# Kernel optimization log

Hardware: AMD Instinct MI355X
Metric: run time of the kernel (lower is better)

Reference implementation:

```python
import jax, jax.numpy as jnp
import numpy as np

B, L, D = 2, 8192, 768
F = 768          # features
ORDER = 2
MAX_LEN = 8192
POS_DIM = 8
INNER = F * (ORDER + 1)  # 2304


def sine_pos_embedding(seq_len, dim=POS_DIM, max_seq_len=MAX_LEN):
    # sine_lin: linearly spaced periods, wrap to negative offsets, include linear coord
    offset = jnp.arange(seq_len)
    offset = jnp.concatenate([offset, offset - seq_len])          # [2L]
    periods = jnp.linspace(4.0, float(max_seq_len), dim // 2)
    freqs = 2.0 * jnp.pi / periods
    phases = jnp.outer(offset, freqs)                              # [2L, dim/2]
    pos_emb = jnp.concatenate((jnp.cos(phases), jnp.sin(phases)), axis=-1)
    pos_emb = jnp.concatenate((offset[:, None] / max_seq_len, pos_emb), axis=-1)
    return pos_emb  # [2L, dim+1]


def fftconv(v, h, bias):
    # v: [B, L, F], h: [1, 2L, F], bias: [1, 1, F]
    seqlen = v.shape[-2]
    n = 2 * seqlen
    h_f = jnp.fft.rfft(h, n=n, axis=-2)
    v_f = jnp.fft.rfft(v, n=n, axis=-2)
    y_f = v_f * h_f / n
    y = jnp.fft.irfft(y_f, axis=-2, n=n, norm='forward')[:, :seqlen, :]
    return y + v * bias


def setup_inputs() -> dict:
    key = jax.random.key(0)
    ks = jax.random.split(key, 13)
    inp = {
        'u': jax.random.normal(ks[0], (B, L, D), jnp.float32),
        'filter_w1': jax.random.normal(ks[1], (POS_DIM + 1, 64), jnp.float32) * (1.0 / np.sqrt(POS_DIM + 1)),
        'filter_b1': jnp.zeros((64,), jnp.float32),
        'filter_w2': jax.random.normal(ks[2], (64, ORDER * F), jnp.float32) * (1.0 / np.sqrt(64)),
        'filter_b2': jnp.zeros((ORDER * F,), jnp.float32),
        'decay': jax.random.uniform(ks[3], (ORDER, F), jnp.float32, 0.5, 4.0),
        'bias': jax.random.normal(ks[4], (ORDER, 1, 1, F), jnp.float32),  # bias_init=1
        'in_proj_w': jax.random.normal(ks[5], (D, INNER), jnp.float32) * 0.02,
        'in_proj_b': jnp.zeros((INNER,), jnp.float32),
        'short_w': jax.random.normal(ks[6], (3, 1, INNER), jnp.float32) * 0.02,  # grouped conv, groups=INNER
        'short_b': jnp.zeros((INNER,), jnp.float32),
        'out_w': jax.random.normal(ks[7], (F, D), jnp.float32) * (1.0 / np.sqrt(F)),
        'out_b': jnp.zeros((D,), jnp.float32),
    }
    return inp


def reference(u, filter_w1, filter_b1, filter_w2, filter_b2, decay, bias,
              in_proj_w, in_proj_b, short_w, short_b, out_w, out_b):
    seq_len = u.shape[-2]
    # --- implicit filter generation from positional embedding ---
    t = sine_pos_embedding(seq_len)[None, :, :]                    # [1, 2L, 9]
    h = jnp.sin(t @ filter_w1 + filter_b1) @ filter_w2 + filter_b2 # [1, 2L, ORDER*F]
    h = h.reshape(1, 2 * seq_len, ORDER, F)
    # --- modulation: exponential decay over normalized position ---
    mod_t = jnp.linspace(0.0, 1.0, MAX_LEN)[:seq_len]
    mod_t = jnp.concatenate([mod_t, jnp.flip(mod_t)])[None, :, None, None]  # [1, 2L, 1, 1]
    h = h * jnp.exp(-mod_t * jnp.abs(decay)[None, None, :, :])
    h = jnp.transpose(h, (2, 0, 1, 3))                             # [ORDER, 1, 2L, F]
    # --- input projection ---
    u = u @ in_proj_w + in_proj_b                                  # [B, L, INNER]
    # --- grouped short conv (depthwise, k=3, SAME) ---
    u = jax.lax.conv_general_dilated(
        u, short_w, window_strides=(1,), padding='SAME',
        dimension_numbers=('NWC', 'WIO', 'NWC'),
        feature_group_count=INNER) + short_b
    # --- hyena recurrence: v <- gate(fftconv(v)) ---
    splits = jnp.split(u, ORDER + 1, axis=-1)
    v, x = splits[0], splits[1:]
    for o in range(ORDER):
        v = fftconv(v, h[o], bias[o])
        v = v * x[o]
    # --- output projection ---
    y = v @ out_w + out_b
    return y
```

## Files before the change

### kernel.cpp

```cpp
#include <hip/hip_runtime.h>
#include <hip/hip_bf16.h>
#include <math.h>

#define L_SEQ 8192
#define NFFT  16384
#define NPAD  16896
#define F_DIM 768
#define D_DIM 768
#define C_IN  2304
#define NORD  2
#define NT    512
#define TWO_PI 6.2831853071795864769f

typedef unsigned short u16;
typedef __attribute__((ext_vector_type(8))) short bf16x8;
typedef __attribute__((ext_vector_type(4))) float f32x4;
struct __align__(8) U16x4 { u16 x, y, z, w; };

__device__ __forceinline__ float bf2f(u16 v) {
  unsigned u = ((unsigned)v) << 16; float f; __builtin_memcpy(&f, &u, 4); return f;
}
__device__ __forceinline__ u16 f2bf(float f) {
  __hip_bfloat16 h = __float2bfloat16(f); u16 r; __builtin_memcpy(&r, &h, 2); return r;
}

__device__ __forceinline__ int PAD(int i) { return i + (i >> 5); }

__device__ __forceinline__ int rev4_14(int p) {
  return ((p & 0x0003) << 12) | ((p & 0x000C) << 8) | ((p & 0x0030) << 4)
       | ( p & 0x00C0       ) | ((p & 0x0300) >> 4) | ((p & 0x0C00) >> 8)
       | ((p & 0x3000) >> 12);
}

__device__ __forceinline__ void rot3(float ang, float& c1, float& s1,
                                     float& c2, float& s2, float& c3, float& s3)
{
  __sincosf(ang, &s1, &c1);
  c2 = c1 * c1 - s1 * s1; s2 = 2.0f * c1 * s1;
  c3 = c1 * c2 - s1 * s2; s3 = c1 * s2 + s1 * c2;
}

__device__ __forceinline__ float conv3b(const u16* __restrict__ row, int t,
                                        float w0, float w1, float w2, float sb)
{
  float l = (t > 0)         ? bf2f(row[t - 1]) : 0.0f;
  float c = bf2f(row[t]);
  float r = (t < L_SEQ - 1) ? bf2f(row[t + 1]) : 0.0f;
  return w0 * l + w1 * c + w2 * r + sb;
}


__device__ __forceinline__ void s1_l2_store(float* zr, float* zi, int g,
    const float yr[4][4], const float yi4[4][4])
{
  const float stw2 = -TWO_PI / 4096.0f;
  float c1, s1, c2, s2, c3, s3;
  rot3(stw2 * (float)g, c1, s1, c2, s2, c3, s3);
  #pragma unroll
  for (int k = 0; k < 4; ++k) {
    float t0r = yr[k][0] + yr[k][2], t0i = yi4[k][0] + yi4[k][2];
    float t1r = yr[k][0] - yr[k][2], t1i = yi4[k][0] - yi4[k][2];
    float t2r = yr[k][1] + yr[k][3], t2i = yi4[k][1] + yi4[k][3];
    float t3r = yr[k][1] - yr[k][3], t3i = yi4[k][1] - yi4[k][3];
    float o0r = t0r + t2r, o0i = t0i + t2i;
    float o1r = t1r + t3i, o1i = t1i - t3r;
    float o2r = t0r - t2r, o2i = t0i - t2i;
    float o3r = t1r - t3i, o3i = t1i + t3r;
    const int i0 = g + (k << 12);
    zr[PAD(i0       )] = o0r;               zi[PAD(i0       )] = o0i;
    zr[PAD(i0 + 1024)] = o1r*c1 - o1i*s1;   zi[PAD(i0 + 1024)] = o1r*s1 + o1i*c1;
    zr[PAD(i0 + 2048)] = o2r*c2 - o2i*s2;   zi[PAD(i0 + 2048)] = o2r*s2 + o2i*c2;
    zr[PAD(i0 + 3072)] = o3r*c3 - o3i*s3;   zi[PAD(i0 + 3072)] = o3r*s3 + o3i*c3;
  }
}

__device__ __forceinline__ void s1_zero_hi(float* zr, float* zi, int g,
    const float xr[2][4], const float xi[2][4])
{
  const float stw1 = -TWO_PI / 16384.0f;
  float yr[4][4], yi4[4][4];
  #pragma unroll
  for (int m = 0; m < 4; ++m) {
    const float x0r = xr[0][m], x0i = xi[0][m];
    const float x1r = xr[1][m], x1i = xi[1][m];
    const float y0r = x0r + x1r, y0i = x0i + x1i;
    const float y1r = x0r + x1i, y1i = x0i - x1r;
    const float y2r = x0r - x1r, y2i = x0i - x1i;
    const float y3r = x0r - x1i, y3i = x0i + x1r;
    float c1, s1, c2, s2, c3, s3;
    rot3(stw1 * (float)(g + (m << 10)), c1, s1, c2, s2, c3, s3);
    yr[0][m] = y0r;               yi4[0][m] = y0i;
    yr[1][m] = y1r*c1 - y1i*s1;   yi4[1][m] = y1r*s1 + y1i*c1;
    yr[2][m] = y2r*c2 - y2i*s2;   yi4[2][m] = y2r*s2 + y2i*c2;
    yr[3][m] = y3r*c3 - y3i*s3;   yi4[3][m] = y3r*s3 + y3i*c3;
  }
  s1_l2_store(zr, zi, g, yr, yi4);
}

template<int LQ0>
__device__ __forceinline__ void fwd_pairs(float* zr, float* zi, int tid)
{
  #pragma unroll
  for (int lq = LQ0; lq >= 4; lq -= 4) {
    const int q  = 1 << lq;
    const int q4 = q >> 2;
    const float stw1 = -TWO_PI / (float)(q << 2);
    const float stw2 = -TWO_PI / (float)q;
    for (int g = tid; g < NFFT / 16; g += NT) {
      const int j    = g & (q4 - 1);
      const int base = ((g >> (lq - 2)) << (lq + 2)) + j;
      float xr[4][4], xi4[4][4];
      #pragma unroll
      for (int k = 0; k < 4; ++k)
        #pragma unroll
        for (int m = 0; m < 4; ++m) {
          const int idx = PAD(base + m * q4 + k * q);
          xr[k][m] = zr[idx]; xi4[k][m] = zi[idx];
        }
      #pragma unroll
      for (int m = 0; m < 4; ++m) {
        float t0r = xr[0][m] + xr[2][m], t0i = xi4[0][m] + xi4[2][m];
        float t1r = xr[0][m] - xr[2][m], t1i = xi4[0][m] - xi4[2][m];
        float t2r = xr[1][m] + xr[3][m], t2i = xi4[1][m] + xi4[3][m];
        float t3r = xr[1][m] - xr[3][m], t3i = xi4[1][m] - xi4[3][m];
        float y0r = t0r + t2r, y0i = t0i + t2i;
        float y1r = t1r + t3i, y1i = t1i - t3r;
        float y2r = t0r - t2r, y2i = t0i - t2i;
        float y3r = t1r - t3i, y3i = t1i + t3r;
        float c1, s1, c2, s2, c3, s3;
        rot3(stw1 * (float)(j + m * q4), c1, s1, c2, s2, c3, s3);
        xr[0][m] = y0r;                xi4[0][m] = y0i;
        xr[1][m] = y1r * c1 - y1i * s1; xi4[1][m] = y1r * s1 + y1i * c1;
        xr[2][m] = y2r * c2 - y2i * s2; xi4[2][m] = y2r * s2 + y2i * c2;
        xr[3][m] = y3r * c3 - y3i * s3; xi4[3][m] = y3r * s3 + y3i * c3;
      }
      float c1, s1, c2, s2, c3, s3;
      rot3(stw2 * (float)j, c1, s1, c2, s2, c3, s3);
      #pragma unroll
      for (int k = 0; k < 4; ++k) {
        float t0r = xr[k][0] + xr[k][2], t0i = xi4[k][0] + xi4[k][2];
        float t1r = xr[k][0] - xr[k][2], t1i = xi4[k][0] - xi4[k][2];
        float t2r = xr[k][1] + xr[k][3], t2i = xi4[k][1] + xi4[k][3];
        float t3r = xr[k][1] - xr[k][3], t3i = xi4[k][1] - xi4[k][3];
        float y0r = t0r + t2r, y0i = t0i + t2i;
        float y1r = t1r + t3i, y1i = t1i - t3r;
        float y2r = t0r - t2r, y2i = t0i - t2i;
        float y3r = t1r - t3i, y3i = t1i + t3r;
        const int i0 = base + k * q;
        zr[PAD(i0         )] = y0r;            zi[PAD(i0         )] = y0i;
        zr[PAD(i0 +     q4)] = y1r*c1 - y1i*s1; zi[PAD(i0 +     q4)] = y1r*s1 + y1i*c1;
        zr[PAD(i0 + 2 * q4)] = y2r*c2 - y2i*s2; zi[PAD(i0 + 2 * q4)] = y2r*s2 + y2i*c2;
        zr[PAD(i0 + 3 * q4)] = y3r*c3 - y3i*s3; zi[PAD(i0 + 3 * q4)] = y3r*s3 + y3i*c3;
      }
    }
    __syncthreads();
  }
}

__device__ __forceinline__ void fused_final_spec_head(float* zr, float* zi,
    const __hip_bfloat162* __restrict__ H, int tid)
{
  for (int b = tid; b < NFFT / 4; b += NT) {
    const int i0 = b << 2;
    const int p  = PAD(i0);
    const float a0r = zr[p],     a0i = zi[p];
    const float a1r = zr[p + 1], a1i = zi[p + 1];
    const float a2r = zr[p + 2], a2i = zi[p + 2];
    const float a3r = zr[p + 3], a3i = zi[p + 3];
    float t0r = a0r + a2r, t0i = a0i + a2i;
    float t1r = a0r - a2r, t1i = a0i - a2i;
    float t2r = a1r + a3r, t2i = a1i + a3i;
    float t3r = a1r - a3r, t3i = a1i - a3i;
    float y0r = t0r + t2r, y0i = t0i + t2i;
    float y1r = t1r + t3i, y1i = t1i - t3r;
    float y2r = t0r - t2r, y2i = t0i - t2i;
    float y3r = t1r - t3i, y3i = t1i + t3r;
    const float4 hq = *(const float4*)&H[i0];
    __hip_bfloat162 h0, h1, h2, h3;
    __builtin_memcpy(&h0, &hq.x, 4); __builtin_memcpy(&h1, &hq.y, 4);
    __builtin_memcpy(&h2, &hq.z, 4); __builtin_memcpy(&h3, &hq.w, 4);
    float hr, hi;
    hr = __bfloat162float(h0.x); hi = __bfloat162float(h0.y);
    const float u0r = y0r*hr - y0i*hi, u0i = y0r*hi + y0i*hr;
    hr = __bfloat162float(h1.x); hi = __bfloat162float(h1.y);
    const float u1r = y1r*hr - y1i*hi, u1i = y1r*hi + y1i*hr;
    hr = __bfloat162float(h2.x); hi = __bfloat162float(h2.y);
    const float u2r = y2r*hr - y2i*hi, u2i = y2r*hi + y2i*hr;
    hr = __bfloat162float(h3.x); hi = __bfloat162float(h3.y);
    const float u3r = y3r*hr - y3i*hi, u3i = y3r*hi + y3i*hr;
    const float e0r = u0r + u2r, e0i = u0i + u2i;
    const float e1r = u0r - u2r, e1i = u0i - u2i;
    const float f0r = u1r + u3r, f0i = u1i + u3i;
    const float f1r = u1r - u3r, f1i = u1i - u3i;
    zr[p]     = e0r + f0r; zi[p]     = e0i + f0i;
    zr[p + 1] = e1r - f1i; zi[p + 1] = e1i + f1r;
    zr[p + 2] = e0r - f0r; zi[p + 2] = e0i - f0i;
    zr[p + 3] = e1r + f1i; zi[p + 3] = e1i - f1r;
  }
  __syncthreads();
}

__device__ __forceinline__ void inv_mid_pairs(float* zr, float* zi, int tid)
{
  #pragma unroll
  for (int lq = 2; lq <= 6; lq += 4) {
    const int q = 1 << lq;
    const int Q = q << 2;
    const float stw1 = TWO_PI / (float)(q << 2);
    const float stw2 = TWO_PI / (float)(Q << 2);
    for (int g = tid; g < NFFT / 16; g += NT) {
      const int j    = g & (q - 1);
      const int base = ((g >> lq) << (lq + 4)) + j;
      float xr[4][4], xi4[4][4];
      #pragma unroll
      for (int k = 0; k < 4; ++k)
        #pragma unroll
        for (int m = 0; m < 4; ++m) {
          const int idx = PAD(base + m * q + k * Q);
          xr[k][m] = zr[idx]; xi4[k][m] = zi[idx];
        }
      {
        float c1, s1, c2, s2, c3, s3;
        rot3(stw1 * (float)j, c1, s1, c2, s2, c3, s3);
        #pragma unroll
        for (int k = 0; k < 4; ++k) {
          float u0r = xr[k][0], u0i = xi4[k][0];
          float u1r = xr[k][1]*c1 - xi4[k][1]*s1, u1i = xr[k][1]*s1 + xi4[k][1]*c1;
          float u2r = xr[k][2]*c2 - xi4[k][2]*s2, u2i = xr[k][2]*s2 + xi4[k][2]*c2;
          float u3r = xr[k][3]*c3 - xi4[k][3]*s3, u3i = xr[k][3]*s3 + xi4[k][3]*c3;
          float e0r = u0r + u2r, e0i = u0i + u2i;
          float e1r = u0r - u2r, e1i = u0i - u2i;
          float f0r = u1r + u3r, f0i = u1i + u3i;
          float f1r = u1r - u3r, f1i = u1i - u3i;
          xr[k][0] = e0r + f0r; xi4[k][0] = e0i + f0i;
          xr[k][1] = e1r - f1i; xi4[k][1] = e1i + f1r;
          xr[k][2] = e0r - f0r; xi4[k][2] = e0i - f0i;
          xr[k][3] = e1r + f1i; xi4[k][3] = e1i - f1r;
        }
      }
      #pragma unroll
      for (int m = 0; m < 4; ++m) {
        float c1, s1, c2, s2, c3, s3;
        rot3(stw2 * (float)(j + m * q), c1, s1, c2, s2, c3, s3);
        float u0r = xr[0][m], u0i = xi4[0][m];
        float u1r = xr[1][m]*c1 - xi4[1][m]*s1, u1i = xr[1][m]*s1 + xi4[1][m]*c1;
        float u2r = xr[2][m]*c2 - xi4[2][m]*s2, u2i = xr[2][m]*s2 + xi4[2][m]*c2;
        float u3r = xr[3][m]*c3 - xi4[3][m]*s3, u3i = xr[3][m]*s3 + xi4[3][m]*c3;
        float e0r = u0r + u2r, e0i = u0i + u2i;
        float e1r = u0r - u2r, e1i = u0i - u2i;
        float f0r = u1r + u3r, f0i = u1i + u3i;
        float f1r = u1r - u3r, f1i = u1i - u3i;
        const int i0 = base + m * q;
        zr[PAD(i0        )] = e0r + f0r; zi[PAD(i0        )] = e0i + f0i;
        zr[PAD(i0 +     Q)] = e1r - f1i; zi[PAD(i0 +     Q)] = e1i + f1r;
        zr[PAD(i0 + 2 * Q)] = e0r - f0r; zi[PAD(i0 + 2 * Q)] = e0i - f0i;
        zr[PAD(i0 + 3 * Q)] = e1r + f1i; zi[PAD(i0 + 3 * Q)] = e1i - f1r;
      }
    }
    __syncthreads();
  }
}

template<bool TO_GLOBAL>
__device__ __forceinline__ void inv_last_gate(float* zr, float* zi,
    const u16* __restrict__ gr0, const u16* __restrict__ gr1,
    float w0, float w1, float w2, float wb, u16* __restrict__ outv, int tid)
{
  const float stw1 = TWO_PI / 4096.0f;
  const float stw2 = TWO_PI / 16384.0f;
  for (int g = tid; g < 1024; g += NT) {
    float xr[4][4], xi4[4][4];
    #pragma unroll
    for (int k = 0; k < 4; ++k)
      #pragma unroll
      for (int m = 0; m < 4; ++m) {
        const int idx = PAD(g + (m << 10) + (k << 12));
        xr[k][m] = zr[idx]; xi4[k][m] = zi[idx];
      }
    {
      float c1, s1, c2, s2, c3, s3;
      rot3(stw1 * (float)g, c1, s1, c2, s2, c3, s3);
      #pragma unroll
      for (int k = 0; k < 4; ++k) {
        float u0r = xr[k][0], u0i = xi4[k][0];
        float u1r = xr[k][1]*c1 - xi4[k][1]*s1, u1i = xr[k][1]*s1 + xi4[k][1]*c1;
        float u2r = xr[k][2]*c2 - xi4[k][2]*s2, u2i = xr[k][2]*s2 + xi4[k][2]*c2;
        float u3r = xr[k][3]*c3 - xi4[k][3]*s3, u3i = xr[k][3]*s3 + xi4[k][3]*c3;
        float e0r = u0r + u2r, e0i = u0i + u2i;
        float e1r = u0r - u2r, e1i = u0i - u2i;
        float f0r = u1r + u3r, f0i = u1i + u3i;
        float f1r = u1r - u3r, f1i = u1i - u3i;
        xr[k][0] = e0r + f0r; xi4[k][0] = e0i + f0i;
        xr[k][1] = e1r - f1i; xi4[k][1] = e1i + f1r;
        xr[k][2] = e0r - f0r; xi4[k][2] = e0i - f0i;
        xr[k][3] = e1r + f1i; xi4[k][3] = e1i - f1r;
      }
    }
    #pragma unroll
    for (int m = 0; m < 4; ++m) {
      float c1, s1, c2, s2, c3, s3;
      rot3(stw2 * (float)(g + (m << 10)), c1, s1, c2, s2, c3, s3);
      float u0r = xr[0][m], u0i = xi4[0][m];
      float u1r = xr[1][m]*c1 - xi4[1][m]*s1, u1i = xr[1][m]*s1 + xi4[1][m]*c1;
      float u2r = xr[2][m]*c2 - xi4[2][m]*s2, u2i = xr[2][m]*s2 + xi4[2][m]*c2;
      float u3r = xr[3][m]*c3 - xi4[3][m]*s3, u3i = xr[3][m]*s3 + xi4[3][m]*c3;
      float e0r = u0r + u2r, e0i = u0i + u2i;
      float e1r = u0r - u2r, e1i = u0i - u2i;
      float f0r = u1r + u3r, f0i = u1i + u3i;
      float f1r = u1r - u3r, f1i = u1i - u3i;
      const int t0 = g + (m << 10);
      const int t1 = t0 + 4096;
      const float o0r = e0r + f0r, o0i = e0i + f0i;
      const float o1r = e1r - f1i, o1i = e1i + f1r;
      const float a0 = conv3b(gr0, t0, w0, w1, w2, wb);
      const float b0 = conv3b(gr1, t0, w0, w1, w2, wb);
      const float a1 = conv3b(gr0, t1, w0, w1, w2, wb);
      const float b1 = conv3b(gr1, t1, w0, w1, w2, wb);
      if (TO_GLOBAL) {
        outv[t0]         = f2bf(o0r * a0);
        outv[L_SEQ + t0] = f2bf(o0i * b0);
        outv[t1]         = f2bf(o1r * a1);
        outv[L_SEQ + t1] = f2bf(o1i * b1);
      } else {
        zr[PAD(t0)] = o0r * a0;  zi[PAD(t0)] = o0i * b0;
        zr[PAD(t1)] = o1r * a1;  zi[PAD(t1)] = o1i * b1;
      }
    }
  }
  if (!TO_GLOBAL) __syncthreads();
}

__global__ __launch_bounds__(256)
void cast_bf16_kernel(const float* __restrict__ in, u16* __restrict__ out, int n4)
{
  int i = blockIdx.x * 256 + threadIdx.x;
  if (i < n4) {
    float4 v = ((const float4*)in)[i];
    U16x4 w; w.x = f2bf(v.x); w.y = f2bf(v.y); w.z = f2bf(v.z); w.w = f2bf(v.w);
    ((U16x4*)out)[i] = w;
  }
}

__global__ __launch_bounds__(256)
void transpose_cast_kernel(const float* __restrict__ in, u16* __restrict__ out,
                           int K, int N)
{
  __shared__ u16 tile[32][33];
  const int n0 = blockIdx.x * 32, k0 = blockIdx.y * 32;
  const int tx = threadIdx.x & 31, ty = threadIdx.x >> 5;
  #pragma unroll
  for (int i = 0; i < 32; i += 8)
    tile[ty + i][tx] = f2bf(in[(size_t)(k0 + ty + i) * N + n0 + tx]);
  __syncthreads();
  #pragma unroll
  for (int i = 0; i < 32; i += 8)
    out[(size_t)(n0 + ty + i) * K + k0 + tx] = tile[tx][ty + i];
}

__global__ __launch_bounds__(256)
void hid_gen_kernel(const float* __restrict__ w1, const float* __restrict__ b1,
                    u16* __restrict__ hidb)
{
  const int tid = threadIdx.x;
  const int r  = tid & 63;
  const int tb = tid >> 6;
  const float w1v0 = w1[r];
  const float b1v  = b1[r];
  float w1c[4], w1s[4];
  #pragma unroll
  for (int p = 0; p < 4; ++p) { w1c[p] = w1[(1 + p) * 64 + r]; w1s[p] = w1[(5 + p) * 64 + r]; }
  const int tau0 = blockIdx.x * 16;
  #pragma unroll
  for (int i = 0; i < 4; ++i) {
    const int tau = tau0 + tb + i * 4;
    const float off = (tau < L_SEQ) ? (float)tau : (float)(tau - NFFT);
    float acc = b1v + off * (1.0f / 8192.0f) * w1v0;
    #pragma unroll
    for (int p = 0; p < 4; ++p) {
      const double period = 4.0 + (8188.0 * p) / 3.0;
      const float freq = (float)(6.283185307179586476925287 / period);
      float sp, cp;
      sincosf(off * freq, &sp, &cp);
      acc += cp * w1c[p] + sp * w1s[p];
    }
    hidb[(size_t)tau * 64 + r] = f2bf(sinf(acc));
  }
}

template<int N_DIM, int K_DIM, int WMODE, int ATRANS = 0, int ASTR = 0>
__global__ __launch_bounds__(256)
void mfma_gemm_kernel(const u16* __restrict__ A, const u16* __restrict__ B,
                      const float* __restrict__ bias, void* __restrict__ Cv,
                      const float* __restrict__ dk)
{
  constexpr int BK = 64;
  __shared__ u16 As[128 * BK];
  __shared__ u16 Bs[128 * BK];
  const int tid  = threadIdx.x;
  const int lane = tid & 63;
  const int wid  = tid >> 6;
  const int m0 = blockIdx.x * 128;
  const int n0 = blockIdx.y * 128;

  const u16* aPtr[4]; const u16* bPtr[4];
  #pragma unroll
  for (int i = 0; i < 4; ++i) {
    const int g = tid + (i << 8);
    if (ATRANS == 0)
      aPtr[i] = A + (size_t)(m0 + (g >> 3)) * K_DIM + ((g & 7) << 3);
    bPtr[i] = B + (size_t)(n0 + (g >> 3)) * K_DIM + ((g & 7) << 3);
  }

  const int wm = (wid & 1) << 6;
  const int wn = (wid >> 1) << 6;
  int aoff[4], boff[4];
  #pragma unroll
  for (int f = 0; f < 4; ++f) {
    aoff[f] = (wm + f * 16 + (lane & 15)) * BK + ((lane >> 4) << 3);
    boff[f] = (wn + f * 16 + (lane & 15)) * BK + ((lane >> 4) << 3);
  }

  f32x4 acc[4][4];
  #pragma unroll
  for (int i = 0; i < 4; ++i)
    #pragma unroll
    for (int j = 0; j < 4; ++j)
      acc[i][j] = (f32x4){0.f, 0.f, 0.f, 0.f};

  for (int k0 = 0; k0 < K_DIM; k0 += BK) {
    if (ATRANS) {
      #pragma unroll
      for (int i = 0; i < 4; ++i) {
        const int g    = tid + (i << 8);
        const int krow = g & 63;
        const int mc   = g >> 6;
        const uint4 v = *(const uint4*)&A[(size_t)(k0 + krow) * ASTR + m0 + mc * 8];
        u16 e[8]; __builtin_memcpy(e, &v, 16);
        #pragma unroll
        for (int q = 0; q < 8; ++q)
          As[(mc * 8 + q) * BK + krow] = e[q];
      }
    } else {
      #pragma unroll
      for (int i = 0; i < 4; ++i) {
        __builtin_amdgcn_global_load_lds(
            (const __attribute__((address_space(1))) void*)aPtr[i],
            (__attribute__((address_space(3))) void*)&As[(((wid << 6) + (i << 8)) << 3)],
            16, 0, 0);
        aPtr[i] += BK;
      }
    }
    #pragma unroll
    for (int i = 0; i < 4; ++i) {
      __builtin_amdgcn_global_load_lds(
          (const __attribute__((address_space(1))) void*)bPtr[i],
          (__attribute__((address_space(3))) void*)&Bs[(((wid << 6) + (i << 8)) << 3)],
          16, 0, 0);
      bPtr[i] += BK;
    }
    __syncthreads();
    #pragma unroll
    for (int kk = 0; kk < 2; ++kk) {
      bf16x8 af[4], bg[4];
      #pragma unroll
      for (int f = 0; f < 4; ++f) af[f] = *(const bf16x8*)&As[aoff[f] + kk * 32];
      #pragma unroll
      for (int f = 0; f < 4; ++f) bg[f] = *(const bf16x8*)&Bs[boff[f] + kk * 32];
      #pragma unroll
      for (int fm = 0; fm < 4; ++fm)
        #pragma unroll
        for (int fn = 0; fn < 4; ++fn)
          acc[fm][fn] = __builtin_amdgcn_mfma_f32_16x16x32_bf16(
              af[fm], bg[fn], acc[fm][fn], 0, 0, 0);
    }
    __syncthreads();
  }

  if (WMODE == 0) {
    u16* C = (u16*)Cv;
    const int b = m0 >> 13;
    const int tbase = (m0 & (L_SEQ - 1)) + wm + ((lane >> 4) << 2);
    #pragma unroll
    for (int fn = 0; fn < 4; ++fn) {
      const int n = n0 + wn + fn * 16 + (lane & 15);
      const float bv = bias[n];
      u16* row = C + ((size_t)b * N_DIM + n) * L_SEQ;
      #pragma unroll
      for (int fm = 0; fm < 4; ++fm) {
        f32x4 v = acc[fm][fn];
        U16x4 w;
        w.x = f2bf(v[0] + bv); w.y = f2bf(v[1] + bv);
        w.z = f2bf(v[2] + bv); w.w = f2bf(v[3] + bv);
        *(U16x4*)&row[tbase + fm * 16] = w;
      }
    }
  } else if (WMODE == 1) {
    float* C = (float*)Cv;
    #pragma unroll
    for (int fn = 0; fn < 4; ++fn) {
      const int n = n0 + wn + fn * 16 + (lane & 15);
      const float bv = bias[n];
      #pragma unroll
      for (int fm = 0; fm < 4; ++fm) {
        const int mb = m0 + wm + fm * 16 + ((lane >> 4) << 2);
        f32x4 v = acc[fm][fn];
        #pragma unroll
        for (int r = 0; r < 4; ++r)
          C[(size_t)(mb + r) * N_DIM + n] = v[r] + bv;
      }
    }
  } else {
    u16* C = (u16*)Cv;
    #pragma unroll
    for (int fn = 0; fn < 4; ++fn) {
      const int n = n0 + wn + fn * 16 + (lane & 15);
      const float bv = bias[n];
      const float ad = fabsf(dk[n]);
      u16* row = C + (size_t)n * (2 * NFFT);
      #pragma unroll
      for (int fm = 0; fm < 4; ++fm) {
        const int mq = m0 + wm + fm * 16 + ((lane >> 4) << 2);
        f32x4 v = acc[fm][fn];
        U16x4 w;
        #pragma unroll
        for (int r = 0; r < 4; ++r) {
          const int t = mq + r;
          const float mt = (t < L_SEQ) ? (float)t * (1.0f / 8191.0f)
                                       : (float)(NFFT - 1 - t) * (1.0f / 8191.0f);
          const float dec = __expf(-mt * ad);
          ((u16*)&w)[r] = f2bf((v[r] + bv) * dec);
        }
        *(U16x4*)&row[mq] = w;
      }
    }
  }
}

__global__ __launch_bounds__(NT)
void filter_fft_kernel(float* __restrict__ hH, const float* __restrict__ bias)
{
  __shared__ float zr[NPAD];
  __shared__ float zi[NPAD];
  const int f = blockIdx.x;
  const int tid = threadIdx.x;
  float* row0 = hH + (size_t)f * NFFT;
  float* row1 = hH + (size_t)(F_DIM + f) * NFFT;
  const u16* h0 = (const u16*)row0;
  const u16* h1 = (const u16*)row1;

  for (int t = tid; t < NFFT; t += NT) {
    zr[PAD(t)] = bf2f(h0[t]);
    zi[PAD(t)] = bf2f(h1[t]);
  }
  __syncthreads();
  fwd_pairs<12>(zr, zi, tid);
  for (int b = tid; b < NFFT / 4; b += NT) {
    const int p = PAD(b << 2);
    const float a0r = zr[p],     a0i = zi[p];
    const float a1r = zr[p + 1], a1i = zi[p + 1];
    const float a2r = zr[p + 2], a2i = zi[p + 2];
    const float a3r = zr[p + 3], a3i = zi[p + 3];
    const float t0r = a0r + a2r, t0i = a0i + a2i;
    const float t1r = a0r - a2r, t1i = a0i - a2i;
    const float t2r = a1r + a3r, t2i = a1i + a3i;
    const float t3r = a1r - a3r, t3i = a1i - a3i;
    zr[p]     = t0r + t2r; zi[p]     = t0i + t2i;
    zr[p + 1] = t1r + t3i; zi[p + 1] = t1i - t3r;
    zr[p + 2] = t0r - t2r; zi[p + 2] = t0i - t2i;
    zr[p + 3] = t1r - t3i; zi[p + 3] = t1i + t3r;
  }
  __syncthreads();
  const float bo0 = bias[f];
  const float bo1 = bias[F_DIM + f];
  const float s = 1.0f / (float)NFFT;
  __hip_bfloat162* o0 = (__hip_bfloat162*)row0;
  __hip_bfloat162* o1 = (__hip_bfloat162*)row1;
  for (int p = tid; p < NFFT; p += NT) {
    const int k  = rev4_14(p);
    const int pb = rev4_14((NFFT - k) & (NFFT - 1));
    const float ar = zr[PAD(p)],  ai = zi[PAD(p)];
    const float br = zr[PAD(pb)], bi = zi[PAD(pb)];
    const float h0r = 0.5f * (ar + br), h0i = 0.5f * (ai - bi);
    const float h1r = 0.5f * (ai + bi), h1i = 0.5f * (br - ar);
    __hip_bfloat162 w0, w1;
    w0.x = __float2bfloat16((h0r + bo0) * s); w0.y = __float2bfloat16(h0i * s);
    w1.x = __float2bfloat16((h1r + bo1) * s); w1.y = __float2bfloat16(h1i * s);
    o0[p] = w0; o1[p] = w1;
  }
}

__global__ __launch_bounds__(NT)
void fftconv_kernel(const u16* __restrict__ up, float* __restrict__ hH,
                    const float* __restrict__ sw, const float* __restrict__ sb)
{
  __shared__ float zr[NPAD];
  __shared__ float zi[NPAD];
  const int f = blockIdx.x;
  const int tid = threadIdx.x;
  float* rowf = hH + (size_t)f * NFFT;
  float* row1 = hH + (size_t)(F_DIM + f) * NFFT;

  const u16* u0 = up + (size_t)(0 * C_IN + f) * L_SEQ;
  const u16* u1 = up + (size_t)(1 * C_IN + f) * L_SEQ;
  const float vw0 = sw[f], vw1 = sw[C_IN + f], vw2 = sw[2 * C_IN + f];
  const float vb = sb[f];

  for (int g = tid; g < 1024; g += NT) {
    float xr[2][4], xi[2][4];
    #pragma unroll
    for (int k = 0; k < 2; ++k)
      #pragma unroll
      for (int m = 0; m < 4; ++m) {
        const int t = g + (m << 10) + (k << 12);
        xr[k][m] = conv3b(u0, t, vw0, vw1, vw2, vb);
        xi[k][m] = conv3b(u1, t, vw0, vw1, vw2, vb);
      }
    s1_zero_hi(zr, zi, g, xr, xi);
  }
  __syncthreads();
  fwd_pairs<8>(zr, zi, tid);
  fused_final_spec_head(zr, zi, (const __hip_bfloat162*)rowf, tid);
  inv_mid_pairs(zr, zi, tid);

  const int c0g = F_DIM + f;
  inv_last_gate<false>(zr, zi,
      up + (size_t)(0 * C_IN + c0g) * L_SEQ,
      up + (size_t)(1 * C_IN + c0g) * L_SEQ,
      sw[c0g], sw[C_IN + c0g], sw[2 * C_IN + c0g], sb[c0g], nullptr, tid);

  for (int g = tid; g < 1024; g += NT) {
    float xr[2][4], xi[2][4];
    #pragma unroll
    for (int k = 0; k < 2; ++k)
      #pragma unroll
      for (int m = 0; m < 4; ++m) {
        const int idx = PAD(g + (m << 10) + (k << 12));
        xr[k][m] = zr[idx]; xi[k][m] = zi[idx];
      }
    s1_zero_hi(zr, zi, g, xr, xi);
  }
  __syncthreads();
  fwd_pairs<8>(zr, zi, tid);
  fused_final_spec_head(zr, zi, (const __hip_bfloat162*)row1, tid);
  inv_mid_pairs(zr, zi, tid);

  const int c1g = 2 * F_DIM + f;
  inv_last_gate<true>(zr, zi,
      up + (size_t)(0 * C_IN + c1g) * L_SEQ,
      up + (size_t)(1 * C_IN + c1g) * L_SEQ,
      sw[c1g], sw[C_IN + c1g], sw[2 * C_IN + c1g], sb[c1g], (u16*)rowf, tid);
}

extern "C" void kernel_launch(void* const* d_in, const int* in_sizes, int n_in,
                              void* d_out, int out_size, void* d_ws, size_t ws_size,
                              hipStream_t stream)
{
  (void)in_sizes; (void)n_in; (void)out_size; (void)ws_size;
  const float* u     = (const float*)d_in[0];
  const float* fw1   = (const float*)d_in[1];
  const float* fb1   = (const float*)d_in[2];
  const float* fw2   = (const float*)d_in[3];
  const float* fb2   = (const float*)d_in[4];
  const float* decay = (const float*)d_in[5];
  const float* bias  = (const float*)d_in[6];
  const float* ipw   = (const float*)d_in[7];
  const float* ipb   = (const float*)d_in[8];
  const float* sw    = (const float*)d_in[9];
  const float* sb    = (const float*)d_in[10];
  const float* ow    = (const float*)d_in[11];
  const float* ob    = (const float*)d_in[12];
  float* out = (float*)d_out;

  char* ws = (char*)d_ws;
  u16*   up_t  = (u16*)(ws);
  float* hH    = (float*)(ws + 75497472);
  u16*   u_bf  = (u16*)(ws + 176160768);
  u16*   ipw_t = (u16*)(ws + 201326592);
  u16*   ow_t  = (u16*)(ws + 204865536);
  u16*   hidb  = (u16*)(ws);
  u16*   w2t   = (u16*)(ws + 2097152);

  cast_bf16_kernel<<<dim3(12288), 256, 0, stream>>>(u, u_bf, (2 * L_SEQ * D_DIM) / 4);
  transpose_cast_kernel<<<dim3(C_IN / 32, D_DIM / 32), 256, 0, stream>>>(ipw, ipw_t, D_DIM, C_IN);
  transpose_cast_kernel<<<dim3(D_DIM / 32, F_DIM / 32), 256, 0, stream>>>(ow, ow_t, F_DIM, D_DIM);

  hid_gen_kernel<<<dim3(NFFT / 16), 256, 0, stream>>>(fw1, fb1, hidb);
  transpose_cast_kernel<<<dim3(1536 / 32, 64 / 32), 256, 0, stream>>>(fw2, w2t, 64, 1536);
  mfma_gemm_kernel<1536, 64, 2><<<dim3(NFFT / 128, 1536 / 128), 256, 0, stream>>>(
      hidb, w2t, fb2, hH, decay);
  filter_fft_kernel<<<dim3(F_DIM), NT, 0, stream>>>(hH, bias);

  mfma_gemm_kernel<C_IN, D_DIM, 0><<<dim3(128, C_IN / 128), 256, 0, stream>>>(u_bf, ipw_t, ipb, up_t, nullptr);
  fftconv_kernel<<<dim3(F_DIM), NT, 0, stream>>>(up_t, hH, sw, sb);
  mfma_gemm_kernel<D_DIM, F_DIM, 1, 1, 2 * NFFT><<<dim3(128, D_DIM / 128), 256, 0, stream>>>(
      (const u16*)hH, ow_t, ob, out, nullptr);
}
```

Baseline: 511.5 us.

## Use twiddle recurrence in FFT, swap GEMM grid order, pack transposed A stores

Several FFT radix stages now call __sincosf once per group and advance the twiddle for later sub-butterflies with a fixed 1/16-turn rotation, replacing three extra sincos calls. The GEMM kernel gains a GSWAP option that swaps the roles of blockIdx.x and blockIdx.y, so consecutive blocks walk the N tiles for the same M rows, aiming for better L2 reuse of A. The transposed-A load path now reads two K rows at once and writes packed 32-bit pairs to LDS, halving the number of LDS store instructions. The twiddle recurrence adds a small rounding drift across the four steps.

Measured after the change: 504.4 us. Within noise of the previous version (-1.4%).

```diff
diff --git a/kernel.cpp b/kernel.cpp
--- a/kernel.cpp
+++ b/kernel.cpp
@@ -11,6 +11,8 @@
 #define NORD  2
 #define NT    512
 #define TWO_PI 6.2831853071795864769f
+#define C16 0.92387953251128675613f
+#define S16 0.38268343236508977172f
 
 typedef unsigned short u16;
 typedef __attribute__((ext_vector_type(8))) short bf16x8;
@@ -38,6 +40,15 @@
   __sincosf(ang, &s1, &c1);
   c2 = c1 * c1 - s1 * s1; s2 = 2.0f * c1 * s1;
   c3 = c1 * c2 - s1 * s2; s3 = c1 * s2 + s1 * c2;
+}
+
+__device__ __forceinline__ void adv_fwd(float& c, float& s) {
+  const float cn = c * C16 + s * S16;
+  s = s * C16 - c * S16; c = cn;
+}
+__device__ __forceinline__ void adv_inv(float& c, float& s) {
+  const float cn = c * C16 - s * S16;
+  s = s * C16 + c * S16; c = cn;
 }
 
 __device__ __forceinline__ float conv3b(const u16* __restrict__ row, int t,
@@ -79,6 +90,8 @@
 {
   const float stw1 = -TWO_PI / 16384.0f;
   float yr[4][4], yi4[4][4];
+  float c1, s1;
+  __sincosf(stw1 * (float)g, &s1, &c1);
   #pragma unroll
   for (int m = 0; m < 4; ++m) {
     const float x0r = xr[0][m], x0i = xi[0][m];
@@ -87,12 +100,13 @@
     const float y1r = x0r + x1i, y1i = x0i - x1r;
     const float y2r = x0r - x1r, y2i = x0i - x1i;
     const float y3r = x0r - x1i, y3i = x0i + x1r;
-    float c1, s1, c2, s2, c3, s3;
-    rot3(stw1 * (float)(g + (m << 10)), c1, s1, c2, s2, c3, s3);
+    const float c2 = c1*c1 - s1*s1, s2 = 2.0f*c1*s1;
+    const float c3 = c1*c2 - s1*s2, s3 = c1*s2 + s1*c2;
     yr[0][m] = y0r;               yi4[0][m] = y0i;
     yr[1][m] = y1r*c1 - y1i*s1;   yi4[1][m] = y1r*s1 + y1i*c1;
     yr[2][m] = y2r*c2 - y2i*s2;   yi4[2][m] = y2r*s2 + y2i*c2;
     yr[3][m] = y3r*c3 - y3i*s3;   yi4[3][m] = y3r*s3 + y3i*c3;
+    adv_fwd(c1, s1);
   }
   s1_l2_store(zr, zi, g, yr, yi4);
 }
@@ -117,6 +131,8 @@
           const int idx = PAD(base + m * q4 + k * q);
           xr[k][m] = zr[idx]; xi4[k][m] = zi[idx];
         }
+      float c1a, s1a;
+      __sincosf(stw1 * (float)j, &s1a, &c1a);
       #pragma unroll
       for (int m = 0; m < 4; ++m) {
         float t0r = xr[0][m] + xr[2][m], t0i = xi4[0][m] + xi4[2][m];
@@ -127,12 +143,13 @@
         float y1r = t1r + t3i, y1i = t1i - t3r;
         float y2r = t0r - t2r, y2i = t0i - t2i;
         float y3r = t1r - t3i, y3i = t1i + t3r;
-        float c1, s1, c2, s2, c3, s3;
-        rot3(stw1 * (float)(j + m * q4), c1, s1, c2, s2, c3, s3);
-        xr[0][m] = y0r;                xi4[0][m] = y0i;
-        xr[1][m] = y1r * c1 - y1i * s1; xi4[1][m] = y1r * s1 + y1i * c1;
-        xr[2][m] = y2r * c2 - y2i * s2; xi4[2][m] = y2r * s2 + y2i * c2;
-        xr[3][m] = y3r * c3 - y3i * s3; xi4[3][m] = y3r * s3 + y3i * c3;
+        const float c2 = c1a*c1a - s1a*s1a, s2 = 2.0f*c1a*s1a;
+        const float c3 = c1a*c2 - s1a*s2, s3 = c1a*s2 + s1a*c2;
+        xr[0][m] = y0r;                  xi4[0][m] = y0i;
+        xr[1][m] = y1r * c1a - y1i * s1a; xi4[1][m] = y1r * s1a + y1i * c1a;
+        xr[2][m] = y2r * c2 - y2i * s2;   xi4[2][m] = y2r * s2 + y2i * c2;
+        xr[3][m] = y3r * c3 - y3i * s3;   xi4[3][m] = y3r * s3 + y3i * c3;
+        adv_fwd(c1a, s1a);
       }
       float c1, s1, c2, s2, c3, s3;
       rot3(stw2 * (float)j, c1, s1, c2, s2, c3, s3);
@@ -238,12 +255,14 @@
           xr[k][3] = e1r + f1i; xi4[k][3] = e1i - f1r;
         }
       }
+      float c1b, s1b;
+      __sincosf(stw2 * (float)j, &s1b, &c1b);
       #pragma unroll
       for (int m = 0; m < 4; ++m) {
-        float c1, s1, c2, s2, c3, s3;
-        rot3(stw2 * (float)(j + m * q), c1, s1, c2, s2, c3, s3);
+        const float c2 = c1b*c1b - s1b*s1b, s2 = 2.0f*c1b*s1b;
+        const float c3 = c1b*c2 - s1b*s2, s3 = c1b*s2 + s1b*c2;
         float u0r = xr[0][m], u0i = xi4[0][m];
-        float u1r = xr[1][m]*c1 - xi4[1][m]*s1, u1i = xr[1][m]*s1 + xi4[1][m]*c1;
+        float u1r = xr[1][m]*c1b - xi4[1][m]*s1b, u1i = xr[1][m]*s1b + xi4[1][m]*c1b;
         float u2r = xr[2][m]*c2 - xi4[2][m]*s2, u2i = xr[2][m]*s2 + xi4[2][m]*c2;
         float u3r = xr[3][m]*c3 - xi4[3][m]*s3, u3i = xr[3][m]*s3 + xi4[3][m]*c3;
         float e0r = u0r + u2r, e0i = u0i + u2i;
@@ -255,6 +274,7 @@
         zr[PAD(i0 +     Q)] = e1r - f1i; zi[PAD(i0 +     Q)] = e1i + f1r;
         zr[PAD(i0 + 2 * Q)] = e0r - f0r; zi[PAD(i0 + 2 * Q)] = e0i - f0i;
         zr[PAD(i0 + 3 * Q)] = e1r + f1i; zi[PAD(i0 + 3 * Q)] = e1i - f1r;
+        adv_inv(c1b, s1b);
       }
     }
     __syncthreads();
@@ -296,12 +316,14 @@
         xr[k][3] = e1r + f1i; xi4[k][3] = e1i - f1r;
       }
     }
+    float c1L, s1L;
+    __sincosf(stw2 * (float)g, &s1L, &c1L);
     #pragma unroll
     for (int m = 0; m < 4; ++m) {
-      float c1, s1, c2, s2, c3, s3;
-      rot3(stw2 * (float)(g + (m << 10)), c1, s1, c2, s2, c3, s3);
+      const float c2 = c1L*c1L - s1L*s1L, s2 = 2.0f*c1L*s1L;
+      const float c3 = c1L*c2 - s1L*s2, s3 = c1L*s2 + s1L*c2;
       float u0r = xr[0][m], u0i = xi4[0][m];
-      float u1r = xr[1][m]*c1 - xi4[1][m]*s1, u1i = xr[1][m]*s1 + xi4[1][m]*c1;
+      float u1r = xr[1][m]*c1L - xi4[1][m]*s1L, u1i = xr[1][m]*s1L + xi4[1][m]*c1L;
       float u2r = xr[2][m]*c2 - xi4[2][m]*s2, u2i = xr[2][m]*s2 + xi4[2][m]*c2;
       float u3r = xr[3][m]*c3 - xi4[3][m]*s3, u3i = xr[3][m]*s3 + xi4[3][m]*c3;
       float e0r = u0r + u2r, e0i = u0i + u2i;
@@ -325,6 +347,7 @@
         zr[PAD(t0)] = o0r * a0;  zi[PAD(t0)] = o0i * b0;
         zr[PAD(t1)] = o1r * a1;  zi[PAD(t1)] = o1i * b1;
       }
+      adv_inv(c1L, s1L);
     }
   }
   if (!TO_GLOBAL) __syncthreads();
@@ -387,7 +410,7 @@
   }
 }
 
-template<int N_DIM, int K_DIM, int WMODE, int ATRANS = 0, int ASTR = 0>
+template<int N_DIM, int K_DIM, int WMODE, int ATRANS = 0, int ASTR = 0, int GSWAP = 0>
 __global__ __launch_bounds__(256)
 void mfma_gemm_kernel(const u16* __restrict__ A, const u16* __restrict__ B,
                       const float* __restrict__ bias, void* __restrict__ Cv,
@@ -399,8 +422,8 @@
   const int tid  = threadIdx.x;
   const int lane = tid & 63;
   const int wid  = tid >> 6;
-  const int m0 = blockIdx.x * 128;
-  const int n0 = blockIdx.y * 128;
+  const int m0 = (GSWAP ? blockIdx.y : blockIdx.x) * 128;
+  const int n0 = (GSWAP ? blockIdx.x : blockIdx.y) * 128;
 
   const u16* aPtr[4]; const u16* bPtr[4];
   #pragma unroll
@@ -430,15 +453,19 @@
   for (int k0 = 0; k0 < K_DIM; k0 += BK) {
     if (ATRANS) {
       #pragma unroll
-      for (int i = 0; i < 4; ++i) {
-        const int g    = tid + (i << 8);
-        const int krow = g & 63;
-        const int mc   = g >> 6;
-        const uint4 v = *(const uint4*)&A[(size_t)(k0 + krow) * ASTR + m0 + mc * 8];
-        u16 e[8]; __builtin_memcpy(e, &v, 16);
+      for (int i = 0; i < 2; ++i) {
+        const int h  = tid + (i << 8);
+        const int kp = h & 31;
+        const int mc = h >> 5;
+        const uint4 v0 = *(const uint4*)&A[(size_t)(k0 + 2 * kp)     * ASTR + m0 + mc * 8];
+        const uint4 v1 = *(const uint4*)&A[(size_t)(k0 + 2 * kp + 1) * ASTR + m0 + mc * 8];
+        u16 e0[8], e1[8];
+        __builtin_memcpy(e0, &v0, 16); __builtin_memcpy(e1, &v1, 16);
         #pragma unroll
-        for (int q = 0; q < 8; ++q)
-          As[(mc * 8 + q) * BK + krow] = e[q];
+        for (int q = 0; q < 8; ++q) {
+          const unsigned pack = (unsigned)e0[q] | ((unsigned)e1[q] << 16);
+          *(unsigned*)&As[(mc * 8 + q) * BK + 2 * kp] = pack;
+        }
       }
     } else {
       #pragma unroll
@@ -686,12 +713,13 @@
 
   hid_gen_kernel<<<dim3(NFFT / 16), 256, 0, stream>>>(fw1, fb1, hidb);
   transpose_cast_kernel<<<dim3(1536 / 32, 64 / 32), 256, 0, stream>>>(fw2, w2t, 64, 1536);
-  mfma_gemm_kernel<1536, 64, 2><<<dim3(NFFT / 128, 1536 / 128), 256, 0, stream>>>(
+  mfma_gemm_kernel<1536, 64, 2, 0, 0, 1><<<dim3(1536 / 128, NFFT / 128), 256, 0, stream>>>(
       hidb, w2t, fb2, hH, decay);
   filter_fft_kernel<<<dim3(F_DIM), NT, 0, stream>>>(hH, bias);
 
-  mfma_gemm_kernel<C_IN, D_DIM, 0><<<dim3(128, C_IN / 128), 256, 0, stream>>>(u_bf, ipw_t, ipb, up_t, nullptr);
+  mfma_gemm_kernel<C_IN, D_DIM, 0, 0, 0, 1><<<dim3(C_IN / 128, 128), 256, 0, stream>>>(
+      u_bf, ipw_t, ipb, up_t, nullptr);
   fftconv_kernel<<<dim3(F_DIM), NT, 0, stream>>>(up_t, hH, sw, sb);
-  mfma_gemm_kernel<D_DIM, F_DIM, 1, 1, 2 * NFFT><<<dim3(128, D_DIM / 128), 256, 0, stream>>>(
+  mfma_gemm_kernel<D_DIM, F_DIM, 1, 1, 2 * NFFT, 1><<<dim3(D_DIM / 128, 128), 256, 0, stream>>>(
       (const u16*)hH, ow_t, ob, out, nullptr);
 }
```
